# Kernel optimization log

Measured on AMD Instinct MI355X. Metric: run time of the kernel, lower is better.

Reference implementation:

```python
import jax, jax.numpy as jnp
import numpy as np

SCALES = (5, 15, 40)


def _hamilton(a, b):
    # a, b: (..., 4) quaternions in [w, x, y, z]
    aw, ax, ay, az = a[..., 0], a[..., 1], a[..., 2], a[..., 3]
    bw, bx, by, bz = b[..., 0], b[..., 1], b[..., 2], b[..., 3]
    return jnp.stack([
        aw * bw - ax * bx - ay * by - az * bz,
        aw * bx + ax * bw + ay * bz - az * by,
        aw * by - ax * bz + ay * bw + az * bx,
        aw * bz + ax * by - ay * bx + az * bw,
    ], axis=-1)


def _bearing_quaternions(xyz):
    # xyz: (B, F, P, 3) -> bearing quaternions (B, F, P, 4)
    bbox_min = xyz.min(axis=2)
    bbox_max = xyz.max(axis=2)
    centroids = (bbox_min + bbox_max) * 0.5  # (B, F, 3)
    d = xyz - centroids[:, :, None, :]
    d = d / jnp.clip(jnp.linalg.norm(d, axis=-1, keepdims=True), 1e-12)
    dot = jnp.clip(d[..., 1], -1.0 + 1e-7, 1.0 - 1e-7)
    half = jnp.arccos(dot) * 0.5
    axis = jnp.stack([d[..., 2], jnp.zeros_like(d[..., 0]), -d[..., 0]], axis=-1)
    axis = axis / jnp.clip(jnp.linalg.norm(axis, axis=-1, keepdims=True), 1e-12)
    s = jnp.sin(half)
    return jnp.stack([jnp.cos(half), axis[..., 0] * s, axis[..., 1] * s, axis[..., 2] * s], axis=-1)


def _torch_lower_median(x):
    flat = jnp.sort(x.reshape(-1))
    return flat[(flat.shape[0] - 1) // 2]


def _bearing_qcc_multiscale(points_4d, num_frames):
    B, F, P, _ = points_4d.shape
    xyz = points_4d[..., :3]  # (B, F, P, 3)
    bq = _bearing_quaternions(xyz)  # (B, F, P, 4)

    # Per-transition relative quaternion q_fwd = q_tgt * conj(q_src), vectorized over T = F-1
    conj_sign = jnp.array([1.0, -1.0, -1.0, -1.0], dtype=points_4d.dtype)
    q_src = bq[:, :-1] * conj_sign  # conj, (B, T, P, 4)
    q_tgt = bq[:, 1:]
    q_fwd = _hamilton(q_tgt, q_src)
    q_fwd = q_fwd / jnp.clip(jnp.linalg.norm(q_fwd, axis=-1, keepdims=True), 1e-12)

    # KNN on source-frame xyz for all transitions at once (topk is sorted desc,
    # so smaller-k neighborhoods are prefixes of the max-k result)
    pts = xyz[:, :-1]  # (B, T, P, 3)
    sq = jnp.sum(pts * pts, axis=-1)  # (B, T, P)
    neg_dist = 2.0 * jnp.einsum('btpc,btqc->btpq', pts, pts) - sq[..., :, None] - sq[..., None, :]
    kmax = max(SCALES)
    _, idx = jax.lax.top_k(neg_dist, kmax)  # (B, T, P, kmax)

    # Gather neighbor quaternions: (B, T, P, kmax, 4)
    b_ix = jnp.arange(B)[:, None, None, None]
    t_ix = jnp.arange(F - 1)[None, :, None, None]
    nbr_q = q_fwd[b_ix, t_ix, idx]

    dots = jnp.abs(jnp.sum(q_fwd[..., None, :] * nbr_q, axis=-1))
    dots = jnp.clip(dots, 0.0, 1.0 - 1e-7)
    geo = 2.0 * jnp.arccos(dots)  # (B, T, P, kmax)

    rigidities = []
    for k in SCALES:
        mean_inc = geo[..., :k].mean(axis=-1).mean(axis=1)  # (B, P)
        scale = jnp.clip(_torch_lower_median(mean_inc), 1e-6)
        rig = jnp.where(mean_inc.max() > 0,
                        jnp.exp(-mean_inc / scale),
                        jnp.ones_like(mean_inc))  # (B, P)
        rig = jnp.broadcast_to(rig[:, None, :], (B, F, P)).reshape(B, 1, F * P)
        rigidities.append(rig)
    return jnp.concatenate(rigidities, axis=1)  # (B, len(SCALES), F*P)


def setup_inputs() -> dict:
    key = jax.random.key(0)
    B, F, P = 2, 8, 2048
    points_4d = jax.random.normal(key, (B, F, P, 4), dtype=jnp.float32)
    return {"points_4d": points_4d, "num_frames": F}


def reference(points_4d, num_frames):
    return _bearing_qcc_multiscale(points_4d, num_frames)
```

## Files before the change

### kernel.cpp

```cpp
#include <hip/hip_runtime.h>
#include <math.h>

typedef unsigned long long u64;
typedef unsigned int u32;

#define B_ 2
#define F_ 8
#define P_ 2048
#define T_ 7
#define ROWS (B_*T_*P_)
#define SENT_OU 0xFFFFFFFFu

#define CED(arr,a,b) do { double _x=arr[a], _y=arr[b]; arr[a]=fmin(_x,_y); arr[b]=fmax(_x,_y); } while(0)

__device__ __forceinline__ void sort8d(double* k) {
  CED(k,0,1); CED(k,2,3); CED(k,4,5); CED(k,6,7);
  CED(k,0,2); CED(k,1,3); CED(k,4,6); CED(k,5,7);
  CED(k,1,2); CED(k,5,6);
  CED(k,0,4); CED(k,1,5); CED(k,2,6); CED(k,3,7);
  CED(k,2,4); CED(k,3,5);
  CED(k,1,2); CED(k,3,4); CED(k,5,6);
}

__device__ __forceinline__ void low8(double* A, const double* Bv) {
#pragma unroll
  for (int i = 0; i < 8; ++i) A[i] = fmin(A[i], Bv[7-i]);
#pragma unroll
  for (int st = 4; st >= 1; st >>= 1) {
#pragma unroll
    for (int i = 0; i < 8; ++i) {
      if ((i & st) == 0) { CED(A, i, i + st); }
    }
  }
}

__device__ __forceinline__ u32 bfly16_min_u32(u32 x) {
  u32 t;
  t = (u32)__builtin_amdgcn_update_dpp((int)x,(int)x,0x0B1,0xF,0xF,false); x = t<x?t:x;
  t = (u32)__builtin_amdgcn_update_dpp((int)x,(int)x,0x04E,0xF,0xF,false); x = t<x?t:x;
  t = (u32)__builtin_amdgcn_update_dpp((int)x,(int)x,0x141,0xF,0xF,false); x = t<x?t:x;
  t = (u32)__builtin_amdgcn_update_dpp((int)x,(int)x,0x140,0xF,0xF,false); x = t<x?t:x;
  return x;
}
__device__ __forceinline__ float bfly16_sum_f32(float x) {
  float t;
  t = __uint_as_float((u32)__builtin_amdgcn_update_dpp((int)__float_as_uint(x),(int)__float_as_uint(x),0x0B1,0xF,0xF,false)); x += t;
  t = __uint_as_float((u32)__builtin_amdgcn_update_dpp((int)__float_as_uint(x),(int)__float_as_uint(x),0x04E,0xF,0xF,false)); x += t;
  t = __uint_as_float((u32)__builtin_amdgcn_update_dpp((int)__float_as_uint(x),(int)__float_as_uint(x),0x141,0xF,0xF,false)); x += t;
  t = __uint_as_float((u32)__builtin_amdgcn_update_dpp((int)__float_as_uint(x),(int)__float_as_uint(x),0x140,0xF,0xF,false)); x += t;
  return x;
}

__global__ __launch_bounds__(256) void kA_bearing(const float4* __restrict__ pts,
                                                  float4* __restrict__ bq,
                                                  float4* __restrict__ pts2) {
  int bf = blockIdx.x;
  const float4* base = pts + (size_t)bf * P_;
  int tid = threadIdx.x;
  float x[8], y[8], z[8];
  float mnx =  INFINITY, mny =  INFINITY, mnz =  INFINITY;
  float mxx = -INFINITY, mxy = -INFINITY, mxz = -INFINITY;
#pragma unroll
  for (int i = 0; i < 8; ++i) {
    float4 v = base[tid + i*256];
    x[i]=v.x; y[i]=v.y; z[i]=v.z;
    mnx=fminf(mnx,v.x); mny=fminf(mny,v.y); mnz=fminf(mnz,v.z);
    mxx=fmaxf(mxx,v.x); mxy=fmaxf(mxy,v.y); mxz=fmaxf(mxz,v.z);
  }
#pragma unroll
  for (int off = 32; off >= 1; off >>= 1) {
    mnx=fminf(mnx,__shfl_xor(mnx,off)); mny=fminf(mny,__shfl_xor(mny,off)); mnz=fminf(mnz,__shfl_xor(mnz,off));
    mxx=fmaxf(mxx,__shfl_xor(mxx,off)); mxy=fmaxf(mxy,__shfl_xor(mxy,off)); mxz=fmaxf(mxz,__shfl_xor(mxz,off));
  }
  __shared__ float red[4][6];
  int wid = tid >> 6, lane = tid & 63;
  if (lane == 0) { red[wid][0]=mnx; red[wid][1]=mny; red[wid][2]=mnz;
                   red[wid][3]=mxx; red[wid][4]=mxy; red[wid][5]=mxz; }
  __syncthreads();
  mnx=fminf(fminf(red[0][0],red[1][0]),fminf(red[2][0],red[3][0]));
  mny=fminf(fminf(red[0][1],red[1][1]),fminf(red[2][1],red[3][1]));
  mnz=fminf(fminf(red[0][2],red[1][2]),fminf(red[2][2],red[3][2]));
  mxx=fmaxf(fmaxf(red[0][3],red[1][3]),fmaxf(red[2][3],red[3][3]));
  mxy=fmaxf(fmaxf(red[0][4],red[1][4]),fmaxf(red[2][4],red[3][4]));
  mxz=fmaxf(fmaxf(red[0][5],red[1][5]),fmaxf(red[2][5],red[3][5]));
  float cx=(mnx+mxx)*0.5f, cy=(mny+mxy)*0.5f, cz=(mnz+mxz)*0.5f;
#pragma unroll
  for (int i = 0; i < 8; ++i) {
    float dx=x[i]-cx, dy=y[i]-cy, dz=z[i]-cz;
    float n = sqrtf(((dx*dx) + dy*dy) + dz*dz);
    n = fmaxf(n, 1e-12f);
    float dxn = dx/n, dyn = dy/n, dzn = dz/n;
    float dotc = fminf(fmaxf(dyn, -0.99999990f), 0.99999990f);
    float half = acosf(dotc) * 0.5f;
    float an = sqrtf(dzn*dzn + dxn*dxn);
    an = fmaxf(an, 1e-12f);
    float axx = dzn/an, axz = (-dxn)/an;
    float s = sinf(half), w = cosf(half);
    bq[(size_t)bf*P_ + tid + i*256] = make_float4(w, axx*s, 0.f, axz*s);
    float qs = fmaf(x[i],x[i], fmaf(y[i],y[i], z[i]*z[i]));
    pts2[(size_t)bf*P_ + tid + i*256] = make_float4(x[i], y[i], z[i], qs);
  }
}

__global__ __launch_bounds__(256) void kB_qfwd(const float4* __restrict__ bq,
                                               float4* __restrict__ qf) {
  int i = blockIdx.x*256 + threadIdx.x;
  int p = i & (P_-1);
  int t = (i >> 11) % T_;
  int b = i / (T_*P_);
  float4 s = bq[((size_t)(b*F_ + t))*P_ + p];
  float4 a = bq[((size_t)(b*F_ + t + 1))*P_ + p];
  float aw=a.x, ax=a.y, ay=a.z, az=a.w;
  float bw=s.x, bx=-s.y, by=-s.z, bz=-s.w;
  float w  = ((aw*bw - ax*bx) - ay*by) - az*bz;
  float xo = ((aw*bx + ax*bw) + ay*bz) - az*by;
  float yo = ((aw*by - ax*bz) + ay*bw) + az*bx;
  float zo = ((aw*bz + ax*by) - ay*bx) + az*bw;
  float n = sqrtf(((w*w + xo*xo) + yo*yo) + zo*zo);
  n = fmaxf(n, 1e-12f);
  qf[i] = make_float4(w/n, xo/n, yo/n, zo/n);
}

__device__ __forceinline__ double mkkey(float4 c, u32 q,
                                        float px, float py, float pz, float ps) {
  float dot = fmaf(px, c.x, fmaf(py, c.y, pz*c.z));
  float nd  = fmaf(-2.f, dot, ps + c.w);
  u32 u = __float_as_uint(nd);
  u32 ou = u ^ (((u32)((int)u >> 31)) | 0x80000000u);
  return __hiloint2double((int)((ou >> 16) | 0x40000000u), (int)((ou << 16) | q));
}
__device__ __forceinline__ u64 mkkey_u(float4 c, u32 q,
                                       float px, float py, float pz, float ps) {
  float dot = fmaf(px, c.x, fmaf(py, c.y, pz*c.z));
  float nd  = fmaf(-2.f, dot, ps + c.w);
  u32 u = __float_as_uint(nd);
  u32 ou = u ^ (((u32)((int)u >> 31)) | 0x80000000u);
  return ((u64)ou << 16) | q;
}

__device__ __forceinline__ void popstep(u32 (&OU)[8], u32 (&IX)[8],
                                        u32& LOU, u32& LIX, u32& CAP, int imod,
                                        int slot, const float4* __restrict__ pbase,
                                        float px, float py, float pz, float ps) {
  if (__any(OU[0] == SENT_OU)) {
    bool need = (OU[0] == SENT_OU);
    u64 lastK = ((u64)LOU << 16) | LIX;
    u64 best = ~0ull;
    for (int j = 0; j < 128; ++j) {
      u32 q = (u32)(j*16 + slot);
      u64 kk = mkkey_u(pbase[q], q, px,py,pz,ps);
      if (kk > lastK && kk < best) best = kk;
    }
    if (need && best != ~0ull) {
      OU[0] = (u32)(best >> 16); IX[0] = (u32)(best & 0xffffu);
      LOU = OU[0]; LIX = IX[0];
    }
  }
  u32 qmin = bfly16_min_u32(OU[0]);
  bool meq = (OU[0] == qmin);
  u32 tt   = meq ? IX[0] : 0xFFFFFFFFu;
  u32 widx = bfly16_min_u32(tt);
  bool iam = meq && (IX[0] == widx);
  CAP = (slot == imod) ? widx : CAP;
#pragma unroll
  for (int jj = 0; jj < 7; ++jj) {
    OU[jj] = iam ? OU[jj+1] : OU[jj];
    IX[jj] = iam ? IX[jj+1] : IX[jj];
  }
  OU[7] = iam ? SENT_OU : OU[7];
}

__global__ __launch_bounds__(256) void kC_select(const float4* __restrict__ pts2,
                                                 const float4* __restrict__ qf,
                                                 float* __restrict__ S) {
  int lane = threadIdx.x & 63;
  int wid  = threadIdx.x >> 6;
  int slot = lane & 15;
  int quarter = lane >> 4;
  int gid = blockIdx.x * 16 + wid * 4;
  int p0 = gid & (P_-1);
  int bt = gid >> 11;
  int t  = bt % T_;
  int b  = bt / T_;
  const float4* pbase = pts2 + (size_t)(b*F_ + t) * P_;

  int prow = p0 + quarter;
  float4 pw = pbase[prow];
  float px=pw.x, py=pw.y, pz=pw.z, ps=pw.w;

  double acc[8];
  {
    double k0[8];
#pragma unroll
    for (int u = 0; u < 8; ++u) { float4 c = pbase[u*16 + slot];
      k0[u] = mkkey(c, (u32)(u*16 + slot), px,py,pz,ps); }
    sort8d(k0);
#pragma unroll
    for (int j = 0; j < 8; ++j) acc[j] = k0[j];
  }
#pragma unroll 2
  for (int batch = 1; batch < 16; ++batch) {
    int qb = batch*128 + slot;
    float4 c[8];
#pragma unroll
    for (int u = 0; u < 8; ++u) c[u] = pbase[qb + u*16];
    double k[8];
#pragma unroll
    for (int u = 0; u < 8; ++u) k[u] = mkkey(c[u], (u32)(qb + u*16), px,py,pz,ps);
    sort8d(k);
    low8(acc, k);
  }

  u32 OU[8], IX[8];
#pragma unroll
  for (int j = 0; j < 8; ++j) {
    u64 bb = (u64)__double_as_longlong(acc[j]);
    OU[j] = (u32)((bb & 0x0000FFFFFFFF0000ull) >> 16);
    IX[j] = (u32)(bb & 0xffffu);
  }
  u32 lou = OU[7], lix = IX[7];
  u32 cap1=0, cap2=0, cap3=0;

#pragma unroll 1
  for (int i = 0; i < 16; ++i)
    popstep(OU, IX, lou, lix, cap1, i, slot, pbase, px,py,pz,ps);
#pragma unroll 1
  for (int i = 0; i < 16; ++i)
    popstep(OU, IX, lou, lix, cap2, i, slot, pbase, px,py,pz,ps);
#pragma unroll 1
  for (int i = 0; i < 8; ++i)
    popstep(OU, IX, lou, lix, cap3, i, slot, pbase, px,py,pz,ps);

  int row = bt*P_ + prow;
  const float4* qbt = qf + (size_t)bt * P_;
  float4 qp = qf[row];

  float4 n; float d;
  n = qbt[cap1]; d = ((qp.x*n.x + qp.y*n.y) + qp.z*n.z) + qp.w*n.w;
  float g1 = 2.f * acosf(fminf(fabsf(d), 0.99999990f));
  n = qbt[cap2]; d = ((qp.x*n.x + qp.y*n.y) + qp.z*n.z) + qp.w*n.w;
  float g2 = 2.f * acosf(fminf(fabsf(d), 0.99999990f));
  n = qbt[cap3]; d = ((qp.x*n.x + qp.y*n.y) + qp.z*n.z) + qp.w*n.w;
  float g3 = (slot < 8) ? 2.f * acosf(fminf(fabsf(d), 0.99999990f)) : 0.f;

  float s40 = bfly16_sum_f32(g1 + g2 + g3);
  float s15 = bfly16_sum_f32((slot < 15) ? g1 : 0.f);
  float s5  = bfly16_sum_f32((slot < 5)  ? g1 : 0.f);

  if (slot == 0) {
    S[0*ROWS + row] = s5  / 5.f;
    S[1*ROWS + row] = s15 / 15.f;
    S[2*ROWS + row] = s40 / 40.f;
  }
}

__global__ __launch_bounds__(1024) void kE_final(const float* __restrict__ S,
                                                 float* __restrict__ out) {
  int k = blockIdx.x;
  int tid = threadIdx.x;
  __shared__ float srt[4096];
  const float* Sk = S + (size_t)k * ROWS;
  float m[4];
#pragma unroll
  for (int u = 0; u < 4; ++u) {
    int j = tid + u*1024;
    int b = j >> 11, p = j & 2047;
    float acc = 0.f;
#pragma unroll
    for (int t = 0; t < 7; ++t) acc += Sk[(b*7 + t)*2048 + p];
    m[u] = acc / 7.f;
    srt[j] = m[u];
  }
  __syncthreads();
  for (int size = 2; size <= 4096; size <<= 1) {
    for (int stride = size >> 1; stride > 0; stride >>= 1) {
      for (int c = tid; c < 2048; c += 1024) {
        int i = 2*c - (c & (stride - 1));
        int j = i + stride;
        bool up = ((i & size) == 0);
        float a = srt[i], bb = srt[j];
        if ((a > bb) == up) { srt[i] = bb; srt[j] = a; }
      }
      __syncthreads();
    }
  }
  float scale = fmaxf(srt[2047], 1e-6f);
  bool pos = srt[4095] > 0.f;
#pragma unroll
  for (int u = 0; u < 4; ++u) {
    int j = tid + u*1024;
    int b = j >> 11, p = j & 2047;
    float r = pos ? expf(-m[u]/scale) : 1.f;
    float* ob = out + ((size_t)(b*3 + k)*8)*2048 + p;
#pragma unroll
    for (int f = 0; f < 8; ++f) ob[f*2048] = r;
  }
}

extern "C" void kernel_launch(void* const* d_in, const int* in_sizes, int n_in,
                              void* d_out, int out_size, void* d_ws, size_t ws_size,
                              hipStream_t stream) {
  (void)in_sizes; (void)n_in; (void)out_size; (void)ws_size;
  const float4* pts = (const float4*)d_in[0];
  float* ws = (float*)d_ws;
  float4* bq   = (float4*)ws;
  float4* qfw  = (float4*)(ws + 131072);
  float*  S    = ws + 131072 + 114688;
  float4* pts2 = (float4*)(ws + 131072 + 114688 + 86016);
  float*  out = (float*)d_out;

  hipLaunchKernelGGL(kA_bearing, dim3(B_*F_), dim3(256), 0, stream, pts, bq, pts2);
  hipLaunchKernelGGL(kB_qfwd,    dim3(ROWS/256), dim3(256), 0, stream, bq, qfw);
  hipLaunchKernelGGL(kC_select,  dim3(ROWS/16), dim3(256), 0, stream, pts2, qfw, S);
  hipLaunchKernelGGL(kE_final,   dim3(3), dim3(1024), 0, stream, S, out);
}
```

Baseline: 129.5 us.

## Split bearing kernel into bbox reduction and wide per-point pass; simplify KNN key

The single bearing kernel, which ran only 16 blocks, is split in two. A small bbox kernel writes per-frame centroids, and a second kernel computes bearing quaternions with one thread per point across 128 blocks, so the transcendental work is spread over many more CUs. The KNN sort key now packs the raw float distance bits and the index directly into a double, dropping the order-preserving transform; the transform is applied only when the key is unpacked. This adds one kernel launch. It relies on sorting doubles by raw float bits, which must still order negative distances correctly.

```diff
diff --git a/kernel.cpp b/kernel.cpp
--- a/kernel.cpp
+++ b/kernel.cpp
@@ -51,19 +51,16 @@
   return x;
 }
 
-__global__ __launch_bounds__(256) void kA_bearing(const float4* __restrict__ pts,
-                                                  float4* __restrict__ bq,
-                                                  float4* __restrict__ pts2) {
+__global__ __launch_bounds__(256) void kA1_bbox(const float4* __restrict__ pts,
+                                                float* __restrict__ cent) {
   int bf = blockIdx.x;
   const float4* base = pts + (size_t)bf * P_;
   int tid = threadIdx.x;
-  float x[8], y[8], z[8];
   float mnx =  INFINITY, mny =  INFINITY, mnz =  INFINITY;
   float mxx = -INFINITY, mxy = -INFINITY, mxz = -INFINITY;
 #pragma unroll
   for (int i = 0; i < 8; ++i) {
     float4 v = base[tid + i*256];
-    x[i]=v.x; y[i]=v.y; z[i]=v.z;
     mnx=fminf(mnx,v.x); mny=fminf(mny,v.y); mnz=fminf(mnz,v.z);
     mxx=fmaxf(mxx,v.x); mxy=fmaxf(mxy,v.y); mxz=fmaxf(mxz,v.z);
   }
@@ -77,29 +74,40 @@
   if (lane == 0) { red[wid][0]=mnx; red[wid][1]=mny; red[wid][2]=mnz;
                    red[wid][3]=mxx; red[wid][4]=mxy; red[wid][5]=mxz; }
   __syncthreads();
-  mnx=fminf(fminf(red[0][0],red[1][0]),fminf(red[2][0],red[3][0]));
-  mny=fminf(fminf(red[0][1],red[1][1]),fminf(red[2][1],red[3][1]));
-  mnz=fminf(fminf(red[0][2],red[1][2]),fminf(red[2][2],red[3][2]));
-  mxx=fmaxf(fmaxf(red[0][3],red[1][3]),fmaxf(red[2][3],red[3][3]));
-  mxy=fmaxf(fmaxf(red[0][4],red[1][4]),fmaxf(red[2][4],red[3][4]));
-  mxz=fmaxf(fmaxf(red[0][5],red[1][5]),fmaxf(red[2][5],red[3][5]));
-  float cx=(mnx+mxx)*0.5f, cy=(mny+mxy)*0.5f, cz=(mnz+mxz)*0.5f;
-#pragma unroll
-  for (int i = 0; i < 8; ++i) {
-    float dx=x[i]-cx, dy=y[i]-cy, dz=z[i]-cz;
-    float n = sqrtf(((dx*dx) + dy*dy) + dz*dz);
-    n = fmaxf(n, 1e-12f);
-    float dxn = dx/n, dyn = dy/n, dzn = dz/n;
-    float dotc = fminf(fmaxf(dyn, -0.99999990f), 0.99999990f);
-    float half = acosf(dotc) * 0.5f;
-    float an = sqrtf(dzn*dzn + dxn*dxn);
-    an = fmaxf(an, 1e-12f);
-    float axx = dzn/an, axz = (-dxn)/an;
-    float s = sinf(half), w = cosf(half);
-    bq[(size_t)bf*P_ + tid + i*256] = make_float4(w, axx*s, 0.f, axz*s);
-    float qs = fmaf(x[i],x[i], fmaf(y[i],y[i], z[i]*z[i]));
-    pts2[(size_t)bf*P_ + tid + i*256] = make_float4(x[i], y[i], z[i], qs);
-  }
+  if (tid == 0) {
+    mnx=fminf(fminf(red[0][0],red[1][0]),fminf(red[2][0],red[3][0]));
+    mny=fminf(fminf(red[0][1],red[1][1]),fminf(red[2][1],red[3][1]));
+    mnz=fminf(fminf(red[0][2],red[1][2]),fminf(red[2][2],red[3][2]));
+    mxx=fmaxf(fmaxf(red[0][3],red[1][3]),fmaxf(red[2][3],red[3][3]));
+    mxy=fmaxf(fmaxf(red[0][4],red[1][4]),fmaxf(red[2][4],red[3][4]));
+    mxz=fmaxf(fmaxf(red[0][5],red[1][5]),fmaxf(red[2][5],red[3][5]));
+    cent[bf*3 + 0] = (mnx+mxx)*0.5f;
+    cent[bf*3 + 1] = (mny+mxy)*0.5f;
+    cent[bf*3 + 2] = (mnz+mxz)*0.5f;
+  }
+}
+
+__global__ __launch_bounds__(256) void kA2_bearing(const float4* __restrict__ pts,
+                                                   const float* __restrict__ cent,
+                                                   float4* __restrict__ bq,
+                                                   float4* __restrict__ pts2) {
+  int idx = blockIdx.x*256 + threadIdx.x;
+  int bf = idx >> 11;
+  float cx = cent[bf*3 + 0], cy = cent[bf*3 + 1], cz = cent[bf*3 + 2];
+  float4 v = pts[idx];
+  float dx=v.x-cx, dy=v.y-cy, dz=v.z-cz;
+  float n = sqrtf(((dx*dx) + dy*dy) + dz*dz);
+  n = fmaxf(n, 1e-12f);
+  float dxn = dx/n, dyn = dy/n, dzn = dz/n;
+  float dotc = fminf(fmaxf(dyn, -0.99999990f), 0.99999990f);
+  float half = acosf(dotc) * 0.5f;
+  float an = sqrtf(dzn*dzn + dxn*dxn);
+  an = fmaxf(an, 1e-12f);
+  float axx = dzn/an, axz = (-dxn)/an;
+  float s = sinf(half), w = cosf(half);
+  bq[idx] = make_float4(w, axx*s, 0.f, axz*s);
+  float qs = fmaf(v.x,v.x, fmaf(v.y,v.y, v.z*v.z));
+  pts2[idx] = make_float4(v.x, v.y, v.z, qs);
 }
 
 __global__ __launch_bounds__(256) void kB_qfwd(const float4* __restrict__ bq,
@@ -125,9 +133,7 @@
                                         float px, float py, float pz, float ps) {
   float dot = fmaf(px, c.x, fmaf(py, c.y, pz*c.z));
   float nd  = fmaf(-2.f, dot, ps + c.w);
-  u32 u = __float_as_uint(nd);
-  u32 ou = u ^ (((u32)((int)u >> 31)) | 0x80000000u);
-  return __hiloint2double((int)((ou >> 16) | 0x40000000u), (int)((ou << 16) | q));
+  return __hiloint2double(__float_as_int(nd), (int)q);
 }
 __device__ __forceinline__ u64 mkkey_u(float4 c, u32 q,
                                        float px, float py, float pz, float ps) {
@@ -215,7 +221,8 @@
 #pragma unroll
   for (int j = 0; j < 8; ++j) {
     u64 bb = (u64)__double_as_longlong(acc[j]);
-    OU[j] = (u32)((bb & 0x0000FFFFFFFF0000ull) >> 16);
+    u32 hi = (u32)(bb >> 32);
+    OU[j] = hi ^ (((u32)((int)hi >> 31)) | 0x80000000u);
     IX[j] = (u32)(bb & 0xffffu);
   }
   u32 lou = OU[7], lix = IX[7];
@@ -307,10 +314,12 @@
   float4* qfw  = (float4*)(ws + 131072);
   float*  S    = ws + 131072 + 114688;
   float4* pts2 = (float4*)(ws + 131072 + 114688 + 86016);
+  float*  cent = ws + 131072 + 114688 + 86016 + 131072;
   float*  out = (float*)d_out;
 
-  hipLaunchKernelGGL(kA_bearing, dim3(B_*F_), dim3(256), 0, stream, pts, bq, pts2);
-  hipLaunchKernelGGL(kB_qfwd,    dim3(ROWS/256), dim3(256), 0, stream, bq, qfw);
-  hipLaunchKernelGGL(kC_select,  dim3(ROWS/16), dim3(256), 0, stream, pts2, qfw, S);
-  hipLaunchKernelGGL(kE_final,   dim3(3), dim3(1024), 0, stream, S, out);
-}
+  hipLaunchKernelGGL(kA1_bbox,    dim3(B_*F_), dim3(256), 0, stream, pts, cent);
+  hipLaunchKernelGGL(kA2_bearing, dim3(B_*F_*P_/256), dim3(256), 0, stream, pts, cent, bq, pts2);
+  hipLaunchKernelGGL(kB_qfwd,     dim3(ROWS/256), dim3(256), 0, stream, bq, qfw);
+  hipLaunchKernelGGL(kC_select,   dim3(ROWS/16), dim3(256), 0, stream, pts2, qfw, S);
+  hipLaunchKernelGGL(kE_final,    dim3(3), dim3(1024), 0, stream, S, out);
+}
```

New measurement: 126.7 us. 1.02x faster.
